# Performance work log

Hardware: AMD Instinct MI355X
Metric: run time of the kernel (lower is better)

Reference implementation:

```python
import jax, jax.numpy as jnp
import numpy as np

NUM_HEADS = 16
SLICE_SIZE = 1024
SCALING = SLICE_SIZE ** 0.5  # module divides by sqrt(slice_size), as written


def setup_inputs() -> dict:
    key = jax.random.key(0)
    ks = jax.random.split(key, 9)
    B, S, D = 4, 2048, SLICE_SIZE
    sc = 0.02
    return {
        "x": jax.random.normal(ks[0], (B, S, D), dtype=jnp.float32),
        "Wq": jax.random.normal(ks[1], (D, D), dtype=jnp.float32) * sc,
        "bq": jax.random.normal(ks[2], (D,), dtype=jnp.float32) * sc,
        "Wk": jax.random.normal(ks[3], (D, D), dtype=jnp.float32) * sc,
        "bk": jax.random.normal(ks[4], (D,), dtype=jnp.float32) * sc,
        "Wv": jax.random.normal(ks[5], (D, D), dtype=jnp.float32) * sc,
        "bv": jax.random.normal(ks[6], (D,), dtype=jnp.float32) * sc,
        "Wp": jax.random.normal(ks[7], (D, D), dtype=jnp.float32) * sc,
        "bp": jax.random.normal(ks[8], (D,), dtype=jnp.float32) * sc,
    }


def _split_heads(t):
    # 'b s (h o) -> b h s o'
    b, s, d = t.shape
    return t.reshape(b, s, NUM_HEADS, d // NUM_HEADS).transpose(0, 2, 1, 3)


def reference(x, Wq, bq, Wk, bk, Wv, bv, Wp, bp):
    q = _split_heads(x @ Wq.T + bq)  # [B,H,S,O]
    k = _split_heads(x @ Wk.T + bk)
    v = _split_heads(x @ Wv.T + bv)
    energy = jnp.einsum('bhqo,bhko->bhqk', q, k)  # full score matrix
    attn = jax.nn.softmax(energy / SCALING, axis=-1)
    # Faithful to source: 'b h q k, b h v o -> b h v o' sums attn over (q,k)
    out = jnp.einsum('bhqk,bhvo->bhvo', attn, v)
    b, h, s, o = out.shape
    out = out.transpose(0, 2, 1, 3).reshape(b, s, h * o)  # 'b h v o -> b v (h o)'
    return out @ Wp.T + bp
```

## Files before the change

### kernel.cpp

```cpp
#include <hip/hip_runtime.h>
#include <cstdint>


typedef unsigned short u16;
typedef __bf16 bf16x8 __attribute__((ext_vector_type(8)));
typedef float f32x4 __attribute__((ext_vector_type(4)));

__device__ __forceinline__ u16 f2bf(float f) {
  unsigned int u = __float_as_uint(f);
  u += 0x7fffu + ((u >> 16) & 1u);
  return (u16)(u >> 16);
}

__device__ __forceinline__ void load16(const void* g, void* l) {
  auto gp = (const __attribute__((address_space(1))) unsigned int*)(uintptr_t)g;
  auto lp = (__attribute__((address_space(3))) unsigned int*)(unsigned int)(uintptr_t)l;
  __builtin_amdgcn_global_load_lds(gp, lp, 16, 0, 0);
}

__global__ void k_prep(const float* __restrict__ x, const float* __restrict__ Wv,
                       const float* __restrict__ bv, const float* __restrict__ Wp,
                       const float* __restrict__ bp, u16* __restrict__ xb,
                       u16* __restrict__ wpb, u16* __restrict__ wvtb,
                       float* __restrict__ cv) {
  __shared__ float tile[32][33];
  const int b = blockIdx.x;
  const int tid = threadIdx.x;
  if (b < 9216) {
    const float* src = (b < 8192) ? x : Wp;
    u16* dst = (b < 8192) ? xb : wpb;
    const long base = (long)((b < 8192) ? b : (b - 8192)) * 1024 + tid * 4;
    const float4 v = *(const float4*)(src + base);
    ushort4 o;
    o.x = f2bf(v.x); o.y = f2bf(v.y); o.z = f2bf(v.z); o.w = f2bf(v.w);
    *(ushort4*)(dst + base) = o;
  } else if (b < 10240) {
    const int tb = b - 9216;
    const int bi = (tb & 31) * 32;
    const int bj = (tb >> 5) * 32;
    const int tx = tid & 31;
    const int ty = tid >> 5;
    for (int r = ty; r < 32; r += 8)
      tile[r][tx] = Wv[(long)(bj + r) * 1024 + bi + tx];
    __syncthreads();
    for (int r = ty; r < 32; r += 8)
      wvtb[(long)(bi + r) * 1024 + bj + tx] = f2bf(tile[tx][r]);
  } else {
    const int row = (b - 10240) * 4 + (tid >> 6);
    const int lane = tid & 63;
    const float* w = Wp + (long)row * 1024;
    float s = 0.f;
    for (int j = lane; j < 1024; j += 64) s += w[j] * bv[j];
    for (int off = 32; off; off >>= 1) s += __shfl_down(s, off, 64);
    if (lane == 0) cv[row] = 2048.f * s + bp[row];
  }
}

template <int MODE>
__global__ __launch_bounds__(MODE == 0 ? 512 : 256) void k_gemm(
    const u16* __restrict__ A, const u16* __restrict__ B, void* __restrict__ OutV,
    const float* __restrict__ bias, int M, int N, int K) {
  constexpr int BM = (MODE == 0) ? 128 : 64;
  constexpr int BN = (MODE == 0) ? 128 : 64;
  constexpr int T  = (MODE == 0) ? 512 : 256;
  constexpr int WTM = (MODE == 0) ? 64 : 32;
  constexpr int WTN = 32;
  constexpr int AccM = WTM / 16;
  constexpr int AccN = WTN / 16;
  constexpr int RPC = T / 8;

  __shared__ u16 As[2][BM * 64];
  __shared__ u16 Bs[2][BN * 64];

  const int tid = threadIdx.x;
  const int lane = tid & 63;
  const int wv = tid >> 6;
  const int waveM = (wv & 1) * WTM;
  const int waveN = (wv >> 1) * WTN;
  const int l15 = lane & 15;
  const int quad = lane >> 4;

  long bm, bn;
  if constexpr (MODE == 0) {
    const int id = blockIdx.x;
    const int xcd = id & 7;
    const int j = id >> 3;
    const int nb = N >> 7;
    const int mPerXcd = M / 128 / 8;
    bm = (long)(xcd * mPerXcd + j / nb) * 128;
    bn = (long)(j % nb) * 128;
  } else {
    bm = (long)(blockIdx.x >> 4) * 64;
    bn = (long)(blockIdx.x & 15) * 64;
  }

  const int rl = tid >> 3;
  const int cs = (tid & 7) ^ (rl & 7);
  const u16* Ag0 = A + (bm + rl) * (long)K + cs * 8;
  const u16* Bg0 = B + (bn + rl) * (long)K + cs * 8;

  const int nT = K >> 6;

  auto STAGE = [&](long k0, int b) {
    u16* Ad = &As[b][0] + tid * 8;
    u16* Bd = &Bs[b][0] + tid * 8;
    load16(Ag0 + k0, Ad);
    load16(Ag0 + k0 + (long)RPC * K, Ad + RPC * 64);
    load16(Bg0 + k0, Bd);
    load16(Bg0 + k0 + (long)RPC * K, Bd + RPC * 64);
  };

  const f32x4 zero = {0.f, 0.f, 0.f, 0.f};
  f32x4 acc[AccM][AccN];
#pragma unroll
  for (int i = 0; i < AccM; ++i)
#pragma unroll
    for (int j = 0; j < AccN; ++j) acc[i][j] = zero;

  const int rq0 = quad ^ (l15 & 7);
  const int rq1 = (4 + quad) ^ (l15 & 7);

  STAGE(0, 0);
  asm volatile("s_waitcnt vmcnt(0)" ::: "memory");
  __builtin_amdgcn_s_barrier();

  int cur = 0;
  for (int t = 0; t < nT; ++t) {
    const bool more = (t + 1) < nT;
    if (more) STAGE((long)(t + 1) << 6, cur ^ 1);
    __builtin_amdgcn_sched_barrier(0);

    const u16* Asb = &As[cur][0];
    const u16* Bsb = &Bs[cur][0];
    bf16x8 af[2][AccM], bg[2][AccN];
#pragma unroll
    for (int i = 0; i < AccM; ++i) {
      const int ra = (waveM + i * 16 + l15) * 64;
      af[0][i] = *(const bf16x8*)(Asb + ra + rq0 * 8);
      af[1][i] = *(const bf16x8*)(Asb + ra + rq1 * 8);
    }
#pragma unroll
    for (int j = 0; j < AccN; ++j) {
      const int rb = (waveN + j * 16 + l15) * 64;
      bg[0][j] = *(const bf16x8*)(Bsb + rb + rq0 * 8);
      bg[1][j] = *(const bf16x8*)(Bsb + rb + rq1 * 8);
    }
    asm volatile("s_waitcnt lgkmcnt(0)" ::: "memory");
    __builtin_amdgcn_sched_barrier(0);

#pragma unroll
    for (int kk = 0; kk < 2; ++kk)
#pragma unroll
      for (int i = 0; i < AccM; ++i)
#pragma unroll
        for (int j = 0; j < AccN; ++j)
          acc[i][j] = __builtin_amdgcn_mfma_f32_16x16x32_bf16(af[kk][i], bg[kk][j],
                                                              acc[i][j], 0, 0, 0);

    if (more) {
      asm volatile("s_waitcnt vmcnt(0)" ::: "memory");
      __builtin_amdgcn_s_barrier();
      cur ^= 1;
    }
  }

#pragma unroll
  for (int i = 0; i < AccM; ++i) {
    const long gm = bm + waveM + i * 16 + quad * 4;
#pragma unroll
    for (int j = 0; j < AccN; ++j) {
      const long gn = bn + waveN + j * 16 + l15;
      if constexpr (MODE == 0) {
        float* outp = (float*)OutV;
        const float bb = bias[gn];
#pragma unroll
        for (int r = 0; r < 4; ++r)
          outp[(gm + r) * N + gn] = acc[i][j][r] + bb;
      } else {
        u16* outp = (u16*)OutV;
#pragma unroll
        for (int r = 0; r < 4; ++r)
          outp[(gm + r) * N + gn] = f2bf(acc[i][j][r] * 2048.f);
      }
    }
  }
}

extern "C" void kernel_launch(void* const* d_in, const int* in_sizes, int n_in,
                              void* d_out, int out_size, void* d_ws, size_t ws_size,
                              hipStream_t stream) {
  const float* x  = (const float*)d_in[0];
  const float* Wv = (const float*)d_in[5];
  const float* bv = (const float*)d_in[6];
  const float* Wp = (const float*)d_in[7];
  const float* bp = (const float*)d_in[8];

  char* ws = (char*)d_ws;
  u16* xb    = (u16*)(ws);
  u16* wpb   = (u16*)(ws + (16u << 20));
  u16* wvtb  = (u16*)(ws + (18u << 20));
  u16* m2b   = (u16*)(ws + (20u << 20));
  float* cv  = (float*)(ws + (22u << 20));

  k_prep<<<10496, 256, 0, stream>>>(x, Wv, bv, Wp, bp, xb, wpb, wvtb, cv);

  k_gemm<1><<<256, 256, 0, stream>>>(wpb, wvtb, m2b, nullptr, 1024, 1024, 1024);

  k_gemm<0><<<512, 512, 0, stream>>>(xb, m2b, d_out, cv, 8192, 1024, 1024);
}
```

Before: 137.7 us.

## Fuse fp32-to-bf16 conversion of x into the main GEMM's A-tile loads

Removes the separate pass that converts x (8192x1024 fp32) to bf16 in the prep kernel and its workspace round trip. The main GEMM now loads fp32 A tiles through registers, converts them to bf16, and writes them into swizzled LDS after the MFMA work of each iteration, while B still uses direct global-to-LDS loads. This saves writing and rereading the bf16 copy of x. In exchange the GEMM reads twice the A bytes, holds more registers, and adds LDS stores before each barrier.

```diff
diff --git a/kernel.cpp b/kernel.cpp
--- a/kernel.cpp
+++ b/kernel.cpp
@@ -12,30 +12,34 @@
   return (u16)(u >> 16);
 }
 
+__device__ __forceinline__ bf16x8 cvt8(float4 a, float4 b) {
+  bf16x8 r;
+  r[0] = (__bf16)a.x; r[1] = (__bf16)a.y; r[2] = (__bf16)a.z; r[3] = (__bf16)a.w;
+  r[4] = (__bf16)b.x; r[5] = (__bf16)b.y; r[6] = (__bf16)b.z; r[7] = (__bf16)b.w;
+  return r;
+}
+
 __device__ __forceinline__ void load16(const void* g, void* l) {
   auto gp = (const __attribute__((address_space(1))) unsigned int*)(uintptr_t)g;
   auto lp = (__attribute__((address_space(3))) unsigned int*)(unsigned int)(uintptr_t)l;
   __builtin_amdgcn_global_load_lds(gp, lp, 16, 0, 0);
 }
 
-__global__ void k_prep(const float* __restrict__ x, const float* __restrict__ Wv,
-                       const float* __restrict__ bv, const float* __restrict__ Wp,
-                       const float* __restrict__ bp, u16* __restrict__ xb,
+__global__ void k_prep(const float* __restrict__ Wv, const float* __restrict__ bv,
+                       const float* __restrict__ Wp, const float* __restrict__ bp,
                        u16* __restrict__ wpb, u16* __restrict__ wvtb,
                        float* __restrict__ cv) {
   __shared__ float tile[32][33];
   const int b = blockIdx.x;
   const int tid = threadIdx.x;
-  if (b < 9216) {
-    const float* src = (b < 8192) ? x : Wp;
-    u16* dst = (b < 8192) ? xb : wpb;
-    const long base = (long)((b < 8192) ? b : (b - 8192)) * 1024 + tid * 4;
-    const float4 v = *(const float4*)(src + base);
+  if (b < 1024) {
+    const long base = (long)b * 1024 + tid * 4;
+    const float4 v = *(const float4*)(Wp + base);
     ushort4 o;
     o.x = f2bf(v.x); o.y = f2bf(v.y); o.z = f2bf(v.z); o.w = f2bf(v.w);
-    *(ushort4*)(dst + base) = o;
-  } else if (b < 10240) {
-    const int tb = b - 9216;
+    *(ushort4*)(wpb + base) = o;
+  } else if (b < 2048) {
+    const int tb = b - 1024;
     const int bi = (tb & 31) * 32;
     const int bj = (tb >> 5) * 32;
     const int tx = tid & 31;
@@ -46,7 +50,7 @@
     for (int r = ty; r < 32; r += 8)
       wvtb[(long)(bi + r) * 1024 + bj + tx] = f2bf(tile[tx][r]);
   } else {
-    const int row = (b - 10240) * 4 + (tid >> 6);
+    const int row = (b - 2048) * 4 + (tid >> 6);
     const int lane = tid & 63;
     const float* w = Wp + (long)row * 1024;
     float s = 0.f;
@@ -58,7 +62,7 @@
 
 template <int MODE>
 __global__ __launch_bounds__(MODE == 0 ? 512 : 256) void k_gemm(
-    const u16* __restrict__ A, const u16* __restrict__ B, void* __restrict__ OutV,
+    const void* __restrict__ Ain, const u16* __restrict__ B, void* __restrict__ OutV,
     const float* __restrict__ bias, int M, int N, int K) {
   constexpr int BM = (MODE == 0) ? 128 : 64;
   constexpr int BN = (MODE == 0) ? 128 : 64;
@@ -67,7 +71,6 @@
   constexpr int WTN = 32;
   constexpr int AccM = WTM / 16;
   constexpr int AccN = WTN / 16;
-  constexpr int RPC = T / 8;
 
   __shared__ u16 As[2][BM * 64];
   __shared__ u16 Bs[2][BN * 64];
@@ -94,21 +97,26 @@
     bn = (long)(blockIdx.x & 15) * 64;
   }
 
+  const int nT = K >> 6;
+
   const int rl = tid >> 3;
   const int cs = (tid & 7) ^ (rl & 7);
-  const u16* Ag0 = A + (bm + rl) * (long)K + cs * 8;
   const u16* Bg0 = B + (bn + rl) * (long)K + cs * 8;
-
-  const int nT = K >> 6;
-
-  auto STAGE = [&](long k0, int b) {
-    u16* Ad = &As[b][0] + tid * 8;
-    u16* Bd = &Bs[b][0] + tid * 8;
-    load16(Ag0 + k0, Ad);
-    load16(Ag0 + k0 + (long)RPC * K, Ad + RPC * 64);
-    load16(Bg0 + k0, Bd);
-    load16(Bg0 + k0 + (long)RPC * K, Bd + RPC * 64);
-  };
+  constexpr int RPC = T / 8;
+
+  const float* Afg = nullptr;
+  const u16* Ag0 = nullptr;
+  int ar = 0, as0 = 0, as1 = 0;
+  if constexpr (MODE == 0) {
+    const float* Af = (const float*)Ain;
+    ar = tid >> 2;
+    const int ap = tid & 3;
+    Afg = Af + (bm + ar) * (long)K + ap * 16;
+    as0 = ((2 * ap)     ^ (ar & 7)) * 8;
+    as1 = ((2 * ap + 1) ^ (ar & 7)) * 8;
+  } else {
+    Ag0 = (const u16*)Ain + (bm + rl) * (long)K + cs * 8;
+  }
 
   const f32x4 zero = {0.f, 0.f, 0.f, 0.f};
   f32x4 acc[AccM][AccN];
@@ -120,14 +128,53 @@
   const int rq0 = quad ^ (l15 & 7);
   const int rq1 = (4 + quad) ^ (l15 & 7);
 
-  STAGE(0, 0);
-  asm volatile("s_waitcnt vmcnt(0)" ::: "memory");
+  if constexpr (MODE == 0) {
+    const float4 v0 = *(const float4*)(Afg + 0);
+    const float4 v1 = *(const float4*)(Afg + 4);
+    const float4 v2 = *(const float4*)(Afg + 8);
+    const float4 v3 = *(const float4*)(Afg + 12);
+    u16* Bd = &Bs[0][0] + tid * 8;
+    load16(Bg0, Bd);
+    load16(Bg0 + (long)RPC * K, Bd + RPC * 64);
+    u16* Aw = &As[0][0] + ar * 64;
+    *(bf16x8*)(Aw + as0) = cvt8(v0, v1);
+    *(bf16x8*)(Aw + as1) = cvt8(v2, v3);
+  } else {
+    u16* Ad = &As[0][0] + tid * 8;
+    u16* Bd = &Bs[0][0] + tid * 8;
+    load16(Ag0, Ad);
+    load16(Ag0 + (long)RPC * K, Ad + RPC * 64);
+    load16(Bg0, Bd);
+    load16(Bg0 + (long)RPC * K, Bd + RPC * 64);
+  }
+  asm volatile("s_waitcnt vmcnt(0) lgkmcnt(0)" ::: "memory");
   __builtin_amdgcn_s_barrier();
 
   int cur = 0;
   for (int t = 0; t < nT; ++t) {
     const bool more = (t + 1) < nT;
-    if (more) STAGE((long)(t + 1) << 6, cur ^ 1);
+    const long k1 = (long)(t + 1) << 6;
+
+    float4 v0, v1, v2, v3;
+    if (more) {
+      if constexpr (MODE == 0) {
+        const float* ag = Afg + k1;
+        v0 = *(const float4*)(ag + 0);
+        v1 = *(const float4*)(ag + 4);
+        v2 = *(const float4*)(ag + 8);
+        v3 = *(const float4*)(ag + 12);
+        u16* Bd = &Bs[cur ^ 1][0] + tid * 8;
+        load16(Bg0 + k1, Bd);
+        load16(Bg0 + k1 + (long)RPC * K, Bd + RPC * 64);
+      } else {
+        u16* Ad = &As[cur ^ 1][0] + tid * 8;
+        u16* Bd = &Bs[cur ^ 1][0] + tid * 8;
+        load16(Ag0 + k1, Ad);
+        load16(Ag0 + k1 + (long)RPC * K, Ad + RPC * 64);
+        load16(Bg0 + k1, Bd);
+        load16(Bg0 + k1 + (long)RPC * K, Bd + RPC * 64);
+      }
+    }
     __builtin_amdgcn_sched_barrier(0);
 
     const u16* Asb = &As[cur][0];
@@ -158,7 +205,12 @@
                                                               acc[i][j], 0, 0, 0);
 
     if (more) {
-      asm volatile("s_waitcnt vmcnt(0)" ::: "memory");
+      if constexpr (MODE == 0) {
+        u16* Aw = &As[cur ^ 1][0] + ar * 64;
+        *(bf16x8*)(Aw + as0) = cvt8(v0, v1);
+        *(bf16x8*)(Aw + as1) = cvt8(v2, v3);
+      }
+      asm volatile("s_waitcnt vmcnt(0) lgkmcnt(0)" ::: "memory");
       __builtin_amdgcn_s_barrier();
       cur ^= 1;
     }
@@ -196,15 +248,14 @@
   const float* bp = (const float*)d_in[8];
 
   char* ws = (char*)d_ws;
-  u16* xb    = (u16*)(ws);
   u16* wpb   = (u16*)(ws + (16u << 20));
   u16* wvtb  = (u16*)(ws + (18u << 20));
   u16* m2b   = (u16*)(ws + (20u << 20));
   float* cv  = (float*)(ws + (22u << 20));
 
-  k_prep<<<10496, 256, 0, stream>>>(x, Wv, bv, Wp, bp, xb, wpb, wvtb, cv);
+  k_prep<<<2304, 256, 0, stream>>>(Wv, bv, Wp, bp, wpb, wvtb, cv);
 
   k_gemm<1><<<256, 256, 0, stream>>>(wpb, wvtb, m2b, nullptr, 1024, 1024, 1024);
 
-  k_gemm<0><<<512, 512, 0, stream>>>(xb, m2b, d_out, cv, 8192, 1024, 1024);
-}
+  k_gemm<0><<<512, 512, 0, stream>>>(x, m2b, d_out, cv, 8192, 1024, 1024);
+}
```

Result: slower. 150.1 us (+8.9%).
